# Performance work log

Hardware: AMD Instinct MI355X
Metric: run time of the kernel (lower is better)

The kernel has to match this reference:

```python
import jax, jax.numpy as jnp
import numpy as np

B, L, H, F, D = 8, 2048, 1024, 256, 3  # batch, seq, d_model, adapter bottleneck, non-news domains
EPS = 1e-6  # annotated-transformer LayerNorm eps


def setup_inputs() -> dict:
    key = jax.random.key(0)
    ks = jax.random.split(key, 6)
    s1 = 1.0 / np.sqrt(H)
    s2 = 1.0 / np.sqrt(F)
    return {
        "x": jax.random.normal(ks[0], (B, L, H), jnp.float32),
        # per-domain LayerNorm params (SublayerConnection.norm)
        "ln_g": jnp.ones((D, H), jnp.float32),
        "ln_b": jnp.zeros((D, H), jnp.float32),
        # per-domain adapter FFN: Linear(H->F), ReLU, Linear(F->H)
        "W1": (jax.random.normal(ks[1], (D, F, H), jnp.float32) * s1),
        "b1": jnp.zeros((D, F), jnp.float32),
        "W2": (jax.random.normal(ks[2], (D, H, F), jnp.float32) * s2),
        "b2": jnp.zeros((D, H), jnp.float32),
        # per-domain gate Linear(2H -> 1), split into the x-half (gu) and adapter-half (gv)
        "gu": (jax.random.normal(ks[3], (D, H), jnp.float32) * s1),
        "gv": (jax.random.normal(ks[4], (D, H), jnp.float32) * s1),
        "gb": jnp.zeros((D,), jnp.float32),
    }


def reference(x, ln_g, ln_b, W1, b1, W2, b2, gu, gv, gb):
    # mix_output=True, used_domain_list=['news','book','bible','iwslt'],
    # target_domain='book' (in list -> no extra pass), dropout=eval (identity).
    mu = jnp.mean(x, axis=-1, keepdims=True)
    sd = jnp.std(x, axis=-1, keepdims=True, ddof=1)  # torch .std default (unbiased)
    xn = (x - mu) / (sd + EPS)                        # shared normalization stats
    # per-domain LayerNorm affine -> [D,B,L,H]
    h = xn[None] * ln_g[:, None, None, :] + ln_b[:, None, None, :]
    # adapter FFN (wo_residual_forward): Linear -> ReLU -> Linear
    mid = jax.nn.relu(jnp.einsum('dblh,dfh->dblf', h, W1) + b1[:, None, None, :])
    a = jnp.einsum('dblf,dhf->dblh', mid, W2) + b2[:, None, None, :]  # [D,B,L,H]
    # gate = sigmoid(Linear([x; a])) with W_gate split as [gu | gv]
    gate = jax.nn.sigmoid(
        jnp.einsum('blh,dh->dbl', x, gu)
        + jnp.einsum('dblh,dh->dbl', a, gv)
        + gb[:, None, None]
    )  # [D,B,L]
    # stacked sum includes 'news' contribution (= x), then outer residual +x:
    return 2.0 * x + jnp.sum(gate[..., None] * a, axis=0)
```

## Files before the change

### kernel.cpp

```cpp
#include <hip/hip_runtime.h>
#include <cstdint>

#define T_TOK 16384
#define H 1024
#define F 256
#define D 3
#define DF 768

typedef unsigned short u16;
typedef __attribute__((ext_vector_type(8))) short short8;
typedef __attribute__((ext_vector_type(4))) float floatx4;

__device__ __forceinline__ u16 f2bf(float f) {
  unsigned u = __float_as_uint(f);
  u += 0x7fff + ((u >> 16) & 1);
  return (u16)(u >> 16);
}
__device__ __forceinline__ float bf2f(u16 s) {
  return __uint_as_float(((unsigned)s) << 16);
}

__device__ __forceinline__ void gload_lds16(const void* g, void* l) {
  __builtin_amdgcn_global_load_lds(
      reinterpret_cast<const __attribute__((address_space(1))) void*>(
          reinterpret_cast<uintptr_t>(g)),
      reinterpret_cast<__attribute__((address_space(3))) void*>(
          reinterpret_cast<uintptr_t>(l)),
      16, 0, 0);
}

__device__ __forceinline__ float block_reduce_256(float v, float* red, int tid) {
  #pragma unroll
  for (int o = 32; o > 0; o >>= 1) v += __shfl_xor(v, o);
  __syncthreads();
  if ((tid & 63) == 0) red[tid >> 6] = v;
  __syncthreads();
  return red[0] + red[1] + red[2] + red[3];
}


__global__ __launch_bounds__(256)
void prep_elem(const float* __restrict__ W1, const float* __restrict__ lng,
               u16* __restrict__ W1p, const float* __restrict__ W2,
               u16* __restrict__ W2r)
{
  int idx = blockIdx.x * 256 + threadIdx.x;
  int stride = gridDim.x * 256;
  for (int i = idx; i < D * F * H; i += stride) {
    int h = i & (H - 1);
    int d = i / (F * H);
    W1p[i] = f2bf(W1[i] * lng[d * H + h]);
  }
  for (int i = idx; i < H * DF; i += stride) {
    int k = i % DF;
    int hh = i / DF;
    int d = k >> 8;
    int f = k & (F - 1);
    W2r[i] = f2bf(W2[((size_t)d * H + hh) * F + f]);
  }
}

__global__ __launch_bounds__(256)
void prep_dots(const float* __restrict__ W1, const float* __restrict__ lnb,
               const float* __restrict__ b1, const float* __restrict__ W2,
               const float* __restrict__ gv, const float* __restrict__ b2,
               const float* __restrict__ gb, float* __restrict__ b1p,
               float* __restrict__ wg, float* __restrict__ cg)
{
  __shared__ float red[4];
  int d = blockIdx.x >> 8;
  int f = blockIdx.x & 255;
  int tid = threadIdx.x;
  float s1 = 0.f, s2 = 0.f, s3 = 0.f;
  for (int h = tid; h < H; h += 256) {
    float w1v = W1[((size_t)d * F + f) * H + h];
    float gvv = gv[d * H + h];
    s1 += lnb[d * H + h] * w1v;
    s2 += W2[((size_t)d * H + h) * F + f] * gvv;
    if (f == 0) s3 += b2[d * H + h] * gvv;
  }
  float S1 = block_reduce_256(s1, red, tid);
  float S2 = block_reduce_256(s2, red, tid);
  if (tid == 0) {
    b1p[d * F + f] = b1[d * F + f] + S1;
    wg[d * F + f] = S2;
  }
  if (f == 0) {
    float S3 = block_reduce_256(s3, red, tid);
    if (tid == 0) cg[d] = gb[d] + S3;
  }
}

__global__ __launch_bounds__(256)
void ln_xu_kernel(const float* __restrict__ x, const float* __restrict__ gu,
                  u16* __restrict__ xn, float* __restrict__ xu)
{
  int t = blockIdx.x;
  int tid = threadIdx.x;
  const float4 xv = *reinterpret_cast<const float4*>(x + (size_t)t * H + tid * 4);
  const float4 g0 = *reinterpret_cast<const float4*>(gu + tid * 4);
  const float4 g1 = *reinterpret_cast<const float4*>(gu + H + tid * 4);
  const float4 g2 = *reinterpret_cast<const float4*>(gu + 2 * H + tid * 4);
  float s  = xv.x + xv.y + xv.z + xv.w;
  float sq = xv.x * xv.x + xv.y * xv.y + xv.z * xv.z + xv.w * xv.w;
  float d0 = xv.x * g0.x + xv.y * g0.y + xv.z * g0.z + xv.w * g0.w;
  float d1 = xv.x * g1.x + xv.y * g1.y + xv.z * g1.z + xv.w * g1.w;
  float d2 = xv.x * g2.x + xv.y * g2.y + xv.z * g2.z + xv.w * g2.w;
  #pragma unroll
  for (int o = 32; o > 0; o >>= 1) {
    s  += __shfl_xor(s, o);  sq += __shfl_xor(sq, o);
    d0 += __shfl_xor(d0, o); d1 += __shfl_xor(d1, o); d2 += __shfl_xor(d2, o);
  }
  __shared__ float red[4][5];
  int w = tid >> 6;
  if ((tid & 63) == 0) {
    red[w][0] = s; red[w][1] = sq; red[w][2] = d0; red[w][3] = d1; red[w][4] = d2;
  }
  __syncthreads();
  float S  = red[0][0] + red[1][0] + red[2][0] + red[3][0];
  float SQ = red[0][1] + red[1][1] + red[2][1] + red[3][1];
  float mu = S * (1.0f / H);
  float var = (SQ - (float)H * mu * mu) * (1.0f / (H - 1));
  float rs = 1.0f / (sqrtf(fmaxf(var, 0.0f)) + 1e-6f);
  ushort4 o4;
  o4.x = f2bf((xv.x - mu) * rs);
  o4.y = f2bf((xv.y - mu) * rs);
  o4.z = f2bf((xv.z - mu) * rs);
  o4.w = f2bf((xv.w - mu) * rs);
  *reinterpret_cast<ushort4*>(xn + (size_t)t * H + tid * 4) = o4;
  if (tid == 0) {
    xu[t]             = red[0][2] + red[1][2] + red[2][2] + red[3][2];
    xu[T_TOK + t]     = red[0][3] + red[1][3] + red[2][3] + red[3][3];
    xu[2 * T_TOK + t] = red[0][4] + red[1][4] + red[2][4] + red[3][4];
  }
}

__global__ __launch_bounds__(192)
void gate_kernel(u16* __restrict__ mid, const float* __restrict__ wg,
                 const float* __restrict__ xu, const float* __restrict__ cg,
                 float* __restrict__ gateOut)
{
  int t = blockIdx.x;
  int tid = threadIdx.x;
  int w = tid >> 6;
  int lane = tid & 63;
  size_t base = (size_t)t * DF + tid * 4;
  ushort4 mv = *reinterpret_cast<const ushort4*>(mid + base);
  float4 wv = *reinterpret_cast<const float4*>(wg + tid * 4);
  float m0 = bf2f(mv.x), m1 = bf2f(mv.y), m2 = bf2f(mv.z), m3 = bf2f(mv.w);
  float dot = m0 * wv.x + m1 * wv.y + m2 * wv.z + m3 * wv.w;
  #pragma unroll
  for (int o = 32; o > 0; o >>= 1) dot += __shfl_xor(dot, o);
  float logit = xu[(size_t)w * T_TOK + t] + dot + cg[w];
  float g = 1.0f / (1.0f + expf(-logit));
  mv.x = f2bf(m0 * g); mv.y = f2bf(m1 * g);
  mv.z = f2bf(m2 * g); mv.w = f2bf(m3 * g);
  *reinterpret_cast<ushort4*>(mid + base) = mv;
  if (lane == 0) gateOut[(size_t)w * T_TOK + t] = g;
}

template <int K, int NLD, int EPI>
__global__ __launch_bounds__(256, 3)
void gemm97(const u16* __restrict__ A, const u16* __restrict__ Bm,
            const float* __restrict__ p0,
            const float* __restrict__ p1,
            const float* __restrict__ p2,
            u16* __restrict__ o16,
            float* __restrict__ o32,
            int nBx, int byX)
{
  constexpr int NT = K / 64;
  extern __shared__ u16 LD[];

  const int tid = threadIdx.x, lane = tid & 63, w = tid >> 6;
  const int wm = w >> 1, wn = w & 1, lr = lane & 15, sl = lane >> 4;

  const int bid = blockIdx.x;
  const int xcd = bid & 7, idx = bid >> 3;
  const int by = xcd * byX + idx / nBx;
  const int bx = idx % nBx;
  const int m0 = by * 128, n0 = bx * 128;

  const u16* Asrc = A + (size_t)m0 * K;
  const u16* Bsrc = Bm + (size_t)n0 * K;

  const int sc8 = ((tid & 7) ^ ((tid >> 3) & 7)) << 3;
  const int grow = tid >> 3;
  const int w512 = w * 512;

  const int rk = lr & 7;
  const int arow = (wm * 64 + lr) * 64;
  const int brow = 8192 + (wn * 64 + lr) * 64;

  floatx4 acc[4][4] = {};
  short8 a[4], b[4];

#define STG(kb_) do { \
    _Pragma("unroll") for (int it_ = 0; it_ < 4; ++it_) \
      gload_lds16(Asrc + (size_t)(it_ * 32 + grow) * K + sc8 + (kb_), \
                  LD + it_ * 2048 + w512); \
    _Pragma("unroll") for (int it_ = 0; it_ < 4; ++it_) \
      gload_lds16(Bsrc + (size_t)(it_ * 32 + grow) * K + sc8 + (kb_), \
                  LD + 8192 + it_ * 2048 + w512); \
  } while (0)
#define LDAB(ks) do { \
    const int ch_ = (((ks) * 4 + sl) ^ rk) << 3; \
    _Pragma("unroll") for (int i_ = 0; i_ < 4; ++i_) { \
      a[i_] = *reinterpret_cast<const short8*>(LD + arow + i_ * 1024 + ch_); \
      b[i_] = *reinterpret_cast<const short8*>(LD + brow + i_ * 1024 + ch_); } \
  } while (0)
#define MMX() do { \
    _Pragma("unroll") for (int mf_ = 0; mf_ < 4; ++mf_) \
      _Pragma("unroll") for (int nf_ = 0; nf_ < 4; ++nf_) \
        acc[mf_][nf_] = __builtin_amdgcn_mfma_f32_16x16x32_bf16( \
            a[mf_], b[nf_], acc[mf_][nf_], 0, 0, 0); } while (0)

  #pragma unroll 1
  for (int t = 0; t < NT; ++t) {
    STG(t * 64);
    __syncthreads();
    LDAB(0); MMX();
    LDAB(1); MMX();
    __syncthreads();
  }

  if constexpr (EPI == 1) {
    float b1v[4];
    #pragma unroll
    for (int nf = 0; nf < 4; ++nf)
      b1v[nf] = p0[n0 + wn * 64 + nf * 16 + lr];
    #pragma unroll
    for (int mf = 0; mf < 4; ++mf)
      #pragma unroll
      for (int i2 = 0; i2 < 4; ++i2) {
        int rl = wm * 64 + mf * 16 + sl * 4 + i2;
        #pragma unroll
        for (int nf = 0; nf < 4; ++nf) {
          int cl = wn * 64 + nf * 16 + lr;
          LD[rl * 136 + cl] = f2bf(fmaxf(acc[mf][nf][i2] + b1v[nf], 0.f));
        }
      }
    __syncthreads();
    #pragma unroll
    for (int it = 0; it < 8; ++it) {
      int q = it * 256 + tid;
      int row = q >> 4, ch = q & 15;
      short8 v = *reinterpret_cast<const short8*>(LD + row * 136 + ch * 8);
      *reinterpret_cast<short8*>(
          &o16[(size_t)(m0 + row) * NLD + n0 + ch * 8]) = v;
    }
  } else {
    float b2v[3][4];
    #pragma unroll
    for (int dd = 0; dd < 3; ++dd)
      #pragma unroll
      for (int nf = 0; nf < 4; ++nf)
        b2v[dd][nf] = p2[dd * H + n0 + wn * 64 + nf * 16 + lr];
    #pragma unroll
    for (int mf = 0; mf < 4; ++mf)
      #pragma unroll
      for (int i2 = 0; i2 < 4; ++i2) {
        int r = m0 + wm * 64 + mf * 16 + sl * 4 + i2;
        float g0 = p1[r], g1 = p1[T_TOK + r], g2 = p1[2 * T_TOK + r];
        const float* xrow = p0 + (size_t)r * H;
        float* orow = o32 + (size_t)r * NLD;
        #pragma unroll
        for (int nf = 0; nf < 4; ++nf) {
          int col = n0 + wn * 64 + nf * 16 + lr;
          orow[col] = acc[mf][nf][i2] + 2.f * xrow[col]
                    + g0 * b2v[0][nf] + g1 * b2v[1][nf] + g2 * b2v[2][nf];
        }
      }
  }
#undef STG
#undef LDAB
#undef MMX
}


extern "C" void kernel_launch(void* const* d_in, const int* in_sizes, int n_in,
                              void* d_out, int out_size, void* d_ws, size_t ws_size,
                              hipStream_t stream) {
  const float* x   = (const float*)d_in[0];
  const float* lng = (const float*)d_in[1];
  const float* lnb = (const float*)d_in[2];
  const float* W1  = (const float*)d_in[3];
  const float* b1  = (const float*)d_in[4];
  const float* W2  = (const float*)d_in[5];
  const float* b2  = (const float*)d_in[6];
  const float* gu  = (const float*)d_in[7];
  const float* gv  = (const float*)d_in[8];
  const float* gb  = (const float*)d_in[9];
  float* out = (float*)d_out;

  char* ws = (char*)d_ws;
  u16* xn   = (u16*)ws;  ws += (size_t)T_TOK * H * 2;
  u16* mid  = (u16*)ws;  ws += (size_t)T_TOK * DF * 2;
  u16* W1p  = (u16*)ws;  ws += (size_t)DF * H * 2;
  u16* W2r  = (u16*)ws;  ws += (size_t)H * DF * 2;
  float* b1p  = (float*)ws;  ws += DF * 4;
  float* wg   = (float*)ws;  ws += DF * 4;
  float* cg   = (float*)ws;  ws += 256;
  float* xu   = (float*)ws;  ws += (size_t)D * T_TOK * 4;
  float* gate = (float*)ws;  ws += (size_t)D * T_TOK * 4;
  (void)ws_size; (void)in_sizes; (void)n_in; (void)out_size;

  hipFuncSetAttribute(reinterpret_cast<const void*>(&gemm97<1024, DF, 1>),
                      hipFuncAttributeMaxDynamicSharedMemorySize, 34816);
  hipFuncSetAttribute(reinterpret_cast<const void*>(&gemm97<768, H, 2>),
                      hipFuncAttributeMaxDynamicSharedMemorySize, 32768);

  prep_elem<<<3072, 256, 0, stream>>>(W1, lng, W1p, W2, W2r);
  prep_dots<<<DF, 256, 0, stream>>>(W1, lnb, b1, W2, gv, b2, gb, b1p, wg, cg);
  ln_xu_kernel<<<T_TOK, 256, 0, stream>>>(x, gu, xn, xu);
  gemm97<1024, DF, 1><<<128 * 6, 256, 34816, stream>>>(
      xn, W1p, b1p, nullptr, nullptr, mid, nullptr, 6, 16);
  gate_kernel<<<T_TOK, 192, 0, stream>>>(mid, wg, xu, cg, gate);
  gemm97<768, H, 2><<<128 * 8, 256, 32768, stream>>>(
      mid, W2r, x, gate, b2, nullptr, out, 8, 16);
}
```

Baseline: 126.2 us.

## Fuse gate computation into GEMM epilogues and drop separate gate kernel

Removes the standalone gate kernel that re-read and rewrote the mid activations. GEMM1's epilogue now computes each tile's partial gate logit dot product and atomically adds it into the logits, which the LayerNorm kernel seeds with the x-half and bias. GEMM2 splits its K loop into three per-domain chunks and applies each sigmoid gate to its partial accumulator. This avoids a full read-modify-write pass over mid, at the cost of atomics, extra accumulator registers in GEMM2, and logits computed from unrounded rather than bf16 values.

```diff
diff --git a/kernel.cpp b/kernel.cpp
--- a/kernel.cpp
+++ b/kernel.cpp
@@ -93,7 +93,8 @@
 
 __global__ __launch_bounds__(256)
 void ln_xu_kernel(const float* __restrict__ x, const float* __restrict__ gu,
-                  u16* __restrict__ xn, float* __restrict__ xu)
+                  const float* __restrict__ cg, u16* __restrict__ xn,
+                  float* __restrict__ lg)
 {
   int t = blockIdx.x;
   int tid = threadIdx.x;
@@ -129,42 +130,18 @@
   o4.w = f2bf((xv.w - mu) * rs);
   *reinterpret_cast<ushort4*>(xn + (size_t)t * H + tid * 4) = o4;
   if (tid == 0) {
-    xu[t]             = red[0][2] + red[1][2] + red[2][2] + red[3][2];
-    xu[T_TOK + t]     = red[0][3] + red[1][3] + red[2][3] + red[3][3];
-    xu[2 * T_TOK + t] = red[0][4] + red[1][4] + red[2][4] + red[3][4];
-  }
-}
-
-__global__ __launch_bounds__(192)
-void gate_kernel(u16* __restrict__ mid, const float* __restrict__ wg,
-                 const float* __restrict__ xu, const float* __restrict__ cg,
-                 float* __restrict__ gateOut)
-{
-  int t = blockIdx.x;
-  int tid = threadIdx.x;
-  int w = tid >> 6;
-  int lane = tid & 63;
-  size_t base = (size_t)t * DF + tid * 4;
-  ushort4 mv = *reinterpret_cast<const ushort4*>(mid + base);
-  float4 wv = *reinterpret_cast<const float4*>(wg + tid * 4);
-  float m0 = bf2f(mv.x), m1 = bf2f(mv.y), m2 = bf2f(mv.z), m3 = bf2f(mv.w);
-  float dot = m0 * wv.x + m1 * wv.y + m2 * wv.z + m3 * wv.w;
-  #pragma unroll
-  for (int o = 32; o > 0; o >>= 1) dot += __shfl_xor(dot, o);
-  float logit = xu[(size_t)w * T_TOK + t] + dot + cg[w];
-  float g = 1.0f / (1.0f + expf(-logit));
-  mv.x = f2bf(m0 * g); mv.y = f2bf(m1 * g);
-  mv.z = f2bf(m2 * g); mv.w = f2bf(m3 * g);
-  *reinterpret_cast<ushort4*>(mid + base) = mv;
-  if (lane == 0) gateOut[(size_t)w * T_TOK + t] = g;
+    lg[t]             = red[0][2] + red[1][2] + red[2][2] + red[3][2] + cg[0];
+    lg[T_TOK + t]     = red[0][3] + red[1][3] + red[2][3] + red[3][3] + cg[1];
+    lg[2 * T_TOK + t] = red[0][4] + red[1][4] + red[2][4] + red[3][4] + cg[2];
+  }
 }
 
 template <int K, int NLD, int EPI>
 __global__ __launch_bounds__(256, 3)
 void gemm97(const u16* __restrict__ A, const u16* __restrict__ Bm,
             const float* __restrict__ p0,
-            const float* __restrict__ p1,
             const float* __restrict__ p2,
+            float* __restrict__ lg,
             u16* __restrict__ o16,
             float* __restrict__ o32,
             int nBx, int byX)
@@ -209,36 +186,72 @@
       a[i_] = *reinterpret_cast<const short8*>(LD + arow + i_ * 1024 + ch_); \
       b[i_] = *reinterpret_cast<const short8*>(LD + brow + i_ * 1024 + ch_); } \
   } while (0)
-#define MMX() do { \
+#define MMX(ACC) do { \
     _Pragma("unroll") for (int mf_ = 0; mf_ < 4; ++mf_) \
       _Pragma("unroll") for (int nf_ = 0; nf_ < 4; ++nf_) \
-        acc[mf_][nf_] = __builtin_amdgcn_mfma_f32_16x16x32_bf16( \
-            a[mf_], b[nf_], acc[mf_][nf_], 0, 0, 0); } while (0)
-
-  #pragma unroll 1
-  for (int t = 0; t < NT; ++t) {
-    STG(t * 64);
-    __syncthreads();
-    LDAB(0); MMX();
-    LDAB(1); MMX();
-    __syncthreads();
-  }
+        ACC[mf_][nf_] = __builtin_amdgcn_mfma_f32_16x16x32_bf16( \
+            a[mf_], b[nf_], ACC[mf_][nf_], 0, 0, 0); } while (0)
 
   if constexpr (EPI == 1) {
-    float b1v[4];
-    #pragma unroll
-    for (int nf = 0; nf < 4; ++nf)
-      b1v[nf] = p0[n0 + wn * 64 + nf * 16 + lr];
+    #pragma unroll 1
+    for (int t = 0; t < NT; ++t) {
+      STG(t * 64);
+      __syncthreads();
+      LDAB(0); MMX(acc);
+      LDAB(1); MMX(acc);
+      __syncthreads();
+    }
+  } else {
+    #pragma unroll 1
+    for (int d = 0; d < 3; ++d) {
+      floatx4 pacc[4][4] = {};
+      #pragma unroll 1
+      for (int kt = 0; kt < 4; ++kt) {
+        STG((d * 4 + kt) * 64);
+        __syncthreads();
+        LDAB(0); MMX(pacc);
+        LDAB(1); MMX(pacc);
+        __syncthreads();
+      }
+      #pragma unroll
+      for (int mf = 0; mf < 4; ++mf)
+        #pragma unroll
+        for (int i2 = 0; i2 < 4; ++i2) {
+          int r = m0 + wm * 64 + mf * 16 + sl * 4 + i2;
+          float l = lg[(size_t)d * T_TOK + r];
+          float g = 1.f / (1.f + expf(-l));
+          #pragma unroll
+          for (int nf = 0; nf < 4; ++nf)
+            acc[mf][nf][i2] += g * pacc[mf][nf][i2];
+        }
+    }
+  }
+
+  if constexpr (EPI == 1) {
+    float b1v[4], wgv[4];
+    #pragma unroll
+    for (int nf = 0; nf < 4; ++nf) {
+      int col = n0 + wn * 64 + nf * 16 + lr;
+      b1v[nf] = p0[col];
+      wgv[nf] = p2[col];
+    }
+    float* red = (float*)(LD + 17408);
     #pragma unroll
     for (int mf = 0; mf < 4; ++mf)
       #pragma unroll
       for (int i2 = 0; i2 < 4; ++i2) {
         int rl = wm * 64 + mf * 16 + sl * 4 + i2;
+        float p = 0.f;
         #pragma unroll
         for (int nf = 0; nf < 4; ++nf) {
           int cl = wn * 64 + nf * 16 + lr;
-          LD[rl * 136 + cl] = f2bf(fmaxf(acc[mf][nf][i2] + b1v[nf], 0.f));
+          float v = fmaxf(acc[mf][nf][i2] + b1v[nf], 0.f);
+          LD[rl * 136 + cl] = f2bf(v);
+          p += v * wgv[nf];
         }
+        p += __shfl_xor(p, 1); p += __shfl_xor(p, 2);
+        p += __shfl_xor(p, 4); p += __shfl_xor(p, 8);
+        if (lr == 0) red[wn * 128 + rl] = p;
       }
     __syncthreads();
     #pragma unroll
@@ -249,6 +262,10 @@
       *reinterpret_cast<short8*>(
           &o16[(size_t)(m0 + row) * NLD + n0 + ch * 8]) = v;
     }
+    const int dgate = bx >> 1;
+    if (tid < 128)
+      atomicAdd(&lg[(size_t)dgate * T_TOK + m0 + tid],
+                red[tid] + red[128 + tid]);
   } else {
     float b2v[3][4];
     #pragma unroll
@@ -261,7 +278,9 @@
       #pragma unroll
       for (int i2 = 0; i2 < 4; ++i2) {
         int r = m0 + wm * 64 + mf * 16 + sl * 4 + i2;
-        float g0 = p1[r], g1 = p1[T_TOK + r], g2 = p1[2 * T_TOK + r];
+        float g0 = 1.f / (1.f + expf(-lg[r]));
+        float g1 = 1.f / (1.f + expf(-lg[T_TOK + r]));
+        float g2 = 1.f / (1.f + expf(-lg[2 * T_TOK + r]));
         const float* xrow = p0 + (size_t)r * H;
         float* orow = o32 + (size_t)r * NLD;
         #pragma unroll
@@ -301,21 +320,19 @@
   float* b1p  = (float*)ws;  ws += DF * 4;
   float* wg   = (float*)ws;  ws += DF * 4;
   float* cg   = (float*)ws;  ws += 256;
-  float* xu   = (float*)ws;  ws += (size_t)D * T_TOK * 4;
-  float* gate = (float*)ws;  ws += (size_t)D * T_TOK * 4;
+  float* lgts = (float*)ws;  ws += (size_t)D * T_TOK * 4;
   (void)ws_size; (void)in_sizes; (void)n_in; (void)out_size;
 
   hipFuncSetAttribute(reinterpret_cast<const void*>(&gemm97<1024, DF, 1>),
-                      hipFuncAttributeMaxDynamicSharedMemorySize, 34816);
+                      hipFuncAttributeMaxDynamicSharedMemorySize, 35840);
   hipFuncSetAttribute(reinterpret_cast<const void*>(&gemm97<768, H, 2>),
                       hipFuncAttributeMaxDynamicSharedMemorySize, 32768);
 
   prep_elem<<<3072, 256, 0, stream>>>(W1, lng, W1p, W2, W2r);
   prep_dots<<<DF, 256, 0, stream>>>(W1, lnb, b1, W2, gv, b2, gb, b1p, wg, cg);
-  ln_xu_kernel<<<T_TOK, 256, 0, stream>>>(x, gu, xn, xu);
-  gemm97<1024, DF, 1><<<128 * 6, 256, 34816, stream>>>(
-      xn, W1p, b1p, nullptr, nullptr, mid, nullptr, 6, 16);
-  gate_kernel<<<T_TOK, 192, 0, stream>>>(mid, wg, xu, cg, gate);
+  ln_xu_kernel<<<T_TOK, 256, 0, stream>>>(x, gu, cg, xn, lgts);
+  gemm97<1024, DF, 1><<<128 * 6, 256, 35840, stream>>>(
+      xn, W1p, b1p, wg, lgts, mid, nullptr, 6, 16);
   gemm97<768, H, 2><<<128 * 8, 256, 32768, stream>>>(
-      mid, W2r, x, gate, b2, nullptr, out, 8, 16);
-}
+      mid, W2r, x, b2, lgts, nullptr, out, 8, 16);
+}
```

Result: slower. 139.8 us (+10.8%).
